# Kernel optimization log

Measured on AMD Instinct MI355X. Metric: run time of the kernel, lower is better.

The kernel has to match this reference:

```python
import jax, jax.numpy as jnp
import numpy as np

SEQ, D_IN, D_OUT = 4096, 1024, 1024


def setup_inputs() -> dict:
    key = jax.random.key(0)
    k_emb, k_q, k_k, k_v = jax.random.split(key, 4)
    # torch Linear stores weight as [out, in]; we keep [in, out] for x @ W
    scale = 1.0 / np.sqrt(D_IN)
    return {
        "embeddings": jax.random.normal(k_emb, (SEQ, D_IN), dtype=jnp.float32),
        "w_query": jax.random.uniform(k_q, (D_IN, D_OUT), dtype=jnp.float32, minval=-scale, maxval=scale),
        "w_key": jax.random.uniform(k_k, (D_IN, D_OUT), dtype=jnp.float32, minval=-scale, maxval=scale),
        "w_value": jax.random.uniform(k_v, (D_IN, D_OUT), dtype=jnp.float32, minval=-scale, maxval=scale),
    }


def reference(embeddings, w_query, w_key, w_value):
    # QKV projections (bias=False)
    q = embeddings @ w_query  # [S, D_out]
    k = embeddings @ w_key    # [S, D_out]
    v = embeddings @ w_value  # [S, D_out]
    inv_sqrt_d = 1.0 / jnp.sqrt(jnp.asarray(k.shape[-1], dtype=q.dtype))
    scores = jnp.einsum("sd,td->st", q, k) * inv_sqrt_d  # [S, S]
    weights = jax.nn.softmax(scores, axis=-1)
    return weights @ v  # [S, D_out]
```

## Files before the change

### kernel.cpp

```cpp
#include <hip/hip_runtime.h>
#include <hip/hip_bf16.h>

typedef unsigned short u16;
typedef __bf16 bf16x8 __attribute__((ext_vector_type(8)));
typedef float f32x4 __attribute__((ext_vector_type(4)));
typedef unsigned short u16x8 __attribute__((ext_vector_type(8)));
typedef unsigned short u16x4 __attribute__((ext_vector_type(4)));

__device__ __forceinline__ float bf2f(u16 u) {
  unsigned x = ((unsigned)u) << 16;
  return __builtin_bit_cast(float, x);
}
__device__ __forceinline__ u16 f2bf(float f) {
  unsigned u = __builtin_bit_cast(unsigned, f);
  u += 0x7fffu + ((u >> 16) & 1u);
  return (u16)(u >> 16);
}

__device__ __forceinline__ void gload16(const u16* g, u16* lds) {
  __builtin_amdgcn_global_load_lds(
      (const __attribute__((address_space(1))) void*)g,
      (__attribute__((address_space(3))) void*)lds,
      16, 0, 0);
}

template <int OUT_MODE, int NX, int BK>
__device__ __forceinline__ void gemm_body(
    const u16* __restrict__ A, int lda,
    const u16* __restrict__ B, int ldb,
    void* __restrict__ C, int ldc, int kt0, int Kc, float cscale,
    u16* As, u16* Bs, int bid)
{
  constexpr int CPR = BK / 8;
  constexpr int RPG = 512 / BK;
  constexpr int IPW = 32 / RPG;

  const int by = (bid & 7) + 8 * (bid / (8 * NX));
  const int bx = (bid >> 3) % NX;
  const int m0 = by * 128, n0 = bx * 128;

  const int t = threadIdx.x;
  const int w = t >> 6, l = t & 63;
  const int srow = l / CPR;
  const int lc = l % CPR;
  const int wm = (w >> 1) * 64, wn = (w & 1) * 64;
  const int fr = l & 15;
  const int q = l >> 4;

  f32x4 acc[4][4] = {};

  for (int kk = 0; kk < Kc; kk += BK) {
    const int kt = kt0 + kk;
    __syncthreads();
#pragma unroll
    for (int j = 0; j < IPW; ++j) {
      const int rr = RPG * (IPW * w + j);
      const int ga = rr + srow;
      const int sch = ((lc ^ (ga & 7))) * 8;
      gload16(A + (size_t)(m0 + ga) * lda + kt + sch, As + rr * BK);
      gload16(B + (size_t)(n0 + ga) * ldb + kt + sch, Bs + rr * BK);
    }
    __syncthreads();

#pragma unroll
    for (int s = 0; s < BK / 32; ++s) {
      const int j = s * 4 + q;
      bf16x8 af[4], bfr[4];
#pragma unroll
      for (int i = 0; i < 4; ++i) {
        const int ra = wm + 16 * i + fr;
        af[i] = *(const bf16x8*)(As + ra * BK + (j ^ (ra & 7)) * 8);
      }
#pragma unroll
      for (int i = 0; i < 4; ++i) {
        const int rb = wn + 16 * i + fr;
        bfr[i] = *(const bf16x8*)(Bs + rb * BK + (j ^ (rb & 7)) * 8);
      }
#pragma unroll
      for (int i = 0; i < 4; ++i)
#pragma unroll
        for (int jj = 0; jj < 4; ++jj)
          acc[i][jj] = __builtin_amdgcn_mfma_f32_16x16x32_bf16(af[i], bfr[jj], acc[i][jj], 0, 0, 0);
    }
  }

  const int er = q * 4;
  const int ec = l & 15;
#pragma unroll
  for (int i = 0; i < 4; ++i)
#pragma unroll
    for (int jj = 0; jj < 4; ++jj)
#pragma unroll
      for (int r = 0; r < 4; ++r) {
        const size_t idx = (size_t)(m0 + wm + 16 * i + er + r) * ldc + (n0 + wn + 16 * jj + ec);
        if (OUT_MODE == 1) ((u16*)C)[idx] = f2bf(acc[i][jj][r] * cscale);
        else               ((float*)C)[idx] = acc[i][jj][r];
      }
}

__global__ __launch_bounds__(256) void gemm_qkv(const u16* __restrict__ A,
                                                const u16* __restrict__ B,
                                                u16* __restrict__ C) {
  __shared__ __align__(16) u16 As[128 * 64], Bs[128 * 64];
  gemm_body<1, 24, 64>(A, 1024, B, 1024, C, 3072, 0, 1024, 1.0f, As, Bs, blockIdx.x);
}

__global__ __launch_bounds__(256) void score_tv(const u16* __restrict__ QKV,
                                                u16* __restrict__ S,
                                                u16* __restrict__ Vt) {
  __shared__ __align__(16) u16 As[128 * 64], Bs[128 * 64];
  const int b = blockIdx.x;
  if (b < 1024) {
    gemm_body<1, 32, 64>(QKV, 3072, QKV + 1024, 3072, S, 4096, 0, 1024,
                         0.03125f, As, Bs, b);
  } else {
    const int v = b - 1024;
    const int c0 = (v & 31) * 32;
    const int r0 = (v >> 5) * 32;
    u16 (*tl)[33] = (u16(*)[33])As;
    const int tx = threadIdx.x & 31, ty0 = threadIdx.x >> 5;
    const u16* Vin = QKV + 2048;
#pragma unroll
    for (int k = 0; k < 4; ++k) {
      const int ty = ty0 + k * 8;
      tl[ty][tx] = Vin[(size_t)(r0 + ty) * 3072 + c0 + tx];
    }
    __syncthreads();
#pragma unroll
    for (int k = 0; k < 4; ++k) {
      const int ty = ty0 + k * 8;
      Vt[(size_t)(c0 + ty) * 4096 + r0 + tx] = tl[tx][ty];
    }
  }
}

__global__ __launch_bounds__(256) void gemm_pv(const u16* __restrict__ S,
                                               const u16* __restrict__ Vt,
                                               float* __restrict__ O0,
                                               float* __restrict__ O1) {
  __shared__ __align__(16) u16 As[128 * 128], Bs[128 * 128];
  float* C = blockIdx.z ? O1 : O0;
  gemm_body<0, 8, 128>(S, 4096, Vt, 4096, C, 1024, blockIdx.z * 2048, 2048,
                       1.0f, As, Bs, blockIdx.x);
}

__global__ __launch_bounds__(256) void reduce_add(float4* __restrict__ out,
                                                  const float4* __restrict__ p) {
  const int i = blockIdx.x * 256 + threadIdx.x;
  float4 a = out[i], b = p[i];
  out[i] = float4{a.x + b.x, a.y + b.y, a.z + b.z, a.w + b.w};
}

__global__ __launch_bounds__(256) void prep(
    const float* __restrict__ E,
    const float* __restrict__ w0, const float* __restrict__ w1,
    const float* __restrict__ w2,
    u16* __restrict__ Ebf, u16* __restrict__ Wt)
{
  int b = blockIdx.x;
  if (b < 4096) {
    const int i = (b * 256 + threadIdx.x) * 4;
    float4 f = *(const float4*)(E + i);
    u16x4 o;
    o.x = f2bf(f.x); o.y = f2bf(f.y); o.z = f2bf(f.z); o.w = f2bf(f.w);
    *(u16x4*)(Ebf + i) = o;
  } else {
    b -= 4096;
    const int which = b >> 10;
    const int tile = b & 1023;
    const float* in = (which == 0) ? w0 : (which == 1) ? w1 : w2;
    u16* o = Wt + (size_t)which * 1024 * 1024;
    const int c0 = (tile & 31) * 32, r0 = (tile >> 5) * 32;
    __shared__ u16 tl[32][33];
    const int tx = threadIdx.x & 31, ty0 = threadIdx.x >> 5;
#pragma unroll
    for (int k = 0; k < 4; ++k) {
      const int ty = ty0 + k * 8;
      tl[ty][tx] = f2bf(in[(size_t)(r0 + ty) * 1024 + c0 + tx]);
    }
    __syncthreads();
#pragma unroll
    for (int k = 0; k < 4; ++k) {
      const int ty = ty0 + k * 8;
      o[(size_t)(c0 + ty) * 1024 + r0 + tx] = tl[tx][ty];
    }
  }
}

__global__ __launch_bounds__(256) void softmax_rows(u16* __restrict__ S) {
  const int N = 4096;
  u16* p = S + (size_t)blockIdx.x * N;
  const int t = threadIdx.x;
  u16x8 u0 = ((const u16x8*)p)[t * 2];
  u16x8 u1 = ((const u16x8*)p)[t * 2 + 1];
  float v[16];
#pragma unroll
  for (int i = 0; i < 8; ++i) v[i] = bf2f(u0[i]);
#pragma unroll
  for (int i = 0; i < 8; ++i) v[8 + i] = bf2f(u1[i]);

  float m = -1e30f;
#pragma unroll
  for (int i = 0; i < 16; ++i) m = fmaxf(m, v[i]);
#pragma unroll
  for (int off = 32; off; off >>= 1) m = fmaxf(m, __shfl_xor(m, off));
  __shared__ float red[8];
  if ((t & 63) == 0) red[t >> 6] = m;
  __syncthreads();
  m = fmaxf(fmaxf(red[0], red[1]), fmaxf(red[2], red[3]));

  float s = 0.f;
#pragma unroll
  for (int i = 0; i < 16; ++i) { v[i] = __expf(v[i] - m); s += v[i]; }
#pragma unroll
  for (int off = 32; off; off >>= 1) s += __shfl_xor(s, off);
  if ((t & 63) == 0) red[4 + (t >> 6)] = s;
  __syncthreads();
  s = (red[4] + red[5]) + (red[6] + red[7]);
  const float inv = 1.0f / s;

  u16x8 o0, o1;
#pragma unroll
  for (int i = 0; i < 8; ++i) o0[i] = f2bf(v[i] * inv);
#pragma unroll
  for (int i = 0; i < 8; ++i) o1[i] = f2bf(v[8 + i] * inv);
  ((u16x8*)p)[t * 2] = o0;
  ((u16x8*)p)[t * 2 + 1] = o1;
}

extern "C" void kernel_launch(void* const* d_in, const int* in_sizes, int n_in,
                              void* d_out, int out_size, void* d_ws, size_t ws_size,
                              hipStream_t stream) {
  const float* E  = (const float*)d_in[0];
  const float* Wq = (const float*)d_in[1];
  const float* Wk = (const float*)d_in[2];
  const float* Wv = (const float*)d_in[3];
  float* Out = (float*)d_out;

  char* w = (char*)d_ws;
  u16* Ebf = (u16*)(w);
  u16* Wt  = (u16*)(w + (size_t)(8u << 20));
  u16* QKV = (u16*)(w + (size_t)(14u << 20));
  u16* Vt  = (u16*)(w + (size_t)(38u << 20));
  u16* S   = (u16*)(w + (size_t)(46u << 20));
  float* P1 = (float*)(w);

  prep<<<7168, 256, 0, stream>>>(E, Wq, Wk, Wv, Ebf, Wt);

  gemm_qkv<<<768, 256, 0, stream>>>(Ebf, Wt, QKV);

  score_tv<<<5120, 256, 0, stream>>>(QKV, S, Vt);

  softmax_rows<<<4096, 256, 0, stream>>>(S);

  gemm_pv<<<dim3(256, 1, 2), 256, 0, stream>>>(S, Vt, Out, P1);
  reduce_add<<<4096, 256, 0, stream>>>((float4*)Out, (const float4*)P1);
}
```

Measured before the change: 220.0 us.

## Replace split-K PV GEMM with 128x64 tiles and drop reduce kernel

Generalizes the GEMM body to a configurable N-tile width and runs the P·V GEMM with 128x64 output tiles over the full K=4096 in 512 blocks, instead of split-K into two partial outputs. This removes the extra partial-sum write, the reduce_add kernel launch and its read-modify-write traffic. In exchange each block runs a longer K loop, and the narrower tile does fewer MFMAs per A-tile load, which lowers arithmetic intensity.

```diff
diff --git a/kernel.cpp b/kernel.cpp
--- a/kernel.cpp
+++ b/kernel.cpp
@@ -24,7 +24,7 @@
       16, 0, 0);
 }
 
-template <int OUT_MODE, int NX, int BK>
+template <int OUT_MODE, int NX, int BK, int BN>
 __device__ __forceinline__ void gemm_body(
     const u16* __restrict__ A, int lda,
     const u16* __restrict__ B, int ldb,
@@ -33,53 +33,62 @@
 {
   constexpr int CPR = BK / 8;
   constexpr int RPG = 512 / BK;
-  constexpr int IPW = 32 / RPG;
+  constexpr int IPA = 32 / RPG;
+  constexpr int IPB = (BN / 4) / RPG;
+  constexpr int NWN = BN / 32;
 
   const int by = (bid & 7) + 8 * (bid / (8 * NX));
   const int bx = (bid >> 3) % NX;
-  const int m0 = by * 128, n0 = bx * 128;
+  const int m0 = by * 128, n0 = bx * BN;
 
   const int t = threadIdx.x;
   const int w = t >> 6, l = t & 63;
   const int srow = l / CPR;
   const int lc = l % CPR;
-  const int wm = (w >> 1) * 64, wn = (w & 1) * 64;
+  const int wm = (w >> 1) * 64;
+  const int wn = (w & 1) * (BN / 2);
   const int fr = l & 15;
   const int q = l >> 4;
 
-  f32x4 acc[4][4] = {};
+  f32x4 acc[4][NWN] = {};
 
   for (int kk = 0; kk < Kc; kk += BK) {
     const int kt = kt0 + kk;
     __syncthreads();
 #pragma unroll
-    for (int j = 0; j < IPW; ++j) {
-      const int rr = RPG * (IPW * w + j);
+    for (int j = 0; j < IPA; ++j) {
+      const int rr = RPG * (IPA * w + j);
       const int ga = rr + srow;
       const int sch = ((lc ^ (ga & 7))) * 8;
       gload16(A + (size_t)(m0 + ga) * lda + kt + sch, As + rr * BK);
-      gload16(B + (size_t)(n0 + ga) * ldb + kt + sch, Bs + rr * BK);
+    }
+#pragma unroll
+    for (int j = 0; j < IPB; ++j) {
+      const int rr = RPG * (IPB * w + j);
+      const int gb = rr + srow;
+      const int sch = ((lc ^ (gb & 7))) * 8;
+      gload16(B + (size_t)(n0 + gb) * ldb + kt + sch, Bs + rr * BK);
     }
     __syncthreads();
 
 #pragma unroll
     for (int s = 0; s < BK / 32; ++s) {
       const int j = s * 4 + q;
-      bf16x8 af[4], bfr[4];
+      bf16x8 af[4], bfr[NWN];
 #pragma unroll
       for (int i = 0; i < 4; ++i) {
         const int ra = wm + 16 * i + fr;
         af[i] = *(const bf16x8*)(As + ra * BK + (j ^ (ra & 7)) * 8);
       }
 #pragma unroll
-      for (int i = 0; i < 4; ++i) {
+      for (int i = 0; i < NWN; ++i) {
         const int rb = wn + 16 * i + fr;
         bfr[i] = *(const bf16x8*)(Bs + rb * BK + (j ^ (rb & 7)) * 8);
       }
 #pragma unroll
       for (int i = 0; i < 4; ++i)
 #pragma unroll
-        for (int jj = 0; jj < 4; ++jj)
+        for (int jj = 0; jj < NWN; ++jj)
           acc[i][jj] = __builtin_amdgcn_mfma_f32_16x16x32_bf16(af[i], bfr[jj], acc[i][jj], 0, 0, 0);
     }
   }
@@ -89,7 +98,7 @@
 #pragma unroll
   for (int i = 0; i < 4; ++i)
 #pragma unroll
-    for (int jj = 0; jj < 4; ++jj)
+    for (int jj = 0; jj < NWN; ++jj)
 #pragma unroll
       for (int r = 0; r < 4; ++r) {
         const size_t idx = (size_t)(m0 + wm + 16 * i + er + r) * ldc + (n0 + wn + 16 * jj + ec);
@@ -102,7 +111,7 @@
                                                 const u16* __restrict__ B,
                                                 u16* __restrict__ C) {
   __shared__ __align__(16) u16 As[128 * 64], Bs[128 * 64];
-  gemm_body<1, 24, 64>(A, 1024, B, 1024, C, 3072, 0, 1024, 1.0f, As, Bs, blockIdx.x);
+  gemm_body<1, 24, 64, 128>(A, 1024, B, 1024, C, 3072, 0, 1024, 1.0f, As, Bs, blockIdx.x);
 }
 
 __global__ __launch_bounds__(256) void score_tv(const u16* __restrict__ QKV,
@@ -111,8 +120,8 @@
   __shared__ __align__(16) u16 As[128 * 64], Bs[128 * 64];
   const int b = blockIdx.x;
   if (b < 1024) {
-    gemm_body<1, 32, 64>(QKV, 3072, QKV + 1024, 3072, S, 4096, 0, 1024,
-                         0.03125f, As, Bs, b);
+    gemm_body<1, 32, 64, 128>(QKV, 3072, QKV + 1024, 3072, S, 4096, 0, 1024,
+                              0.03125f, As, Bs, b);
   } else {
     const int v = b - 1024;
     const int c0 = (v & 31) * 32;
@@ -136,19 +145,10 @@
 
 __global__ __launch_bounds__(256) void gemm_pv(const u16* __restrict__ S,
                                                const u16* __restrict__ Vt,
-                                               float* __restrict__ O0,
-                                               float* __restrict__ O1) {
-  __shared__ __align__(16) u16 As[128 * 128], Bs[128 * 128];
-  float* C = blockIdx.z ? O1 : O0;
-  gemm_body<0, 8, 128>(S, 4096, Vt, 4096, C, 1024, blockIdx.z * 2048, 2048,
-                       1.0f, As, Bs, blockIdx.x);
-}
-
-__global__ __launch_bounds__(256) void reduce_add(float4* __restrict__ out,
-                                                  const float4* __restrict__ p) {
-  const int i = blockIdx.x * 256 + threadIdx.x;
-  float4 a = out[i], b = p[i];
-  out[i] = float4{a.x + b.x, a.y + b.y, a.z + b.z, a.w + b.w};
+                                               float* __restrict__ O) {
+  __shared__ __align__(16) u16 As[128 * 128], Bs[64 * 128];
+  gemm_body<0, 16, 128, 64>(S, 4096, Vt, 4096, O, 1024, 0, 4096,
+                            1.0f, As, Bs, blockIdx.x);
 }
 
 __global__ __launch_bounds__(256) void prep(
@@ -243,7 +243,6 @@
   u16* QKV = (u16*)(w + (size_t)(14u << 20));
   u16* Vt  = (u16*)(w + (size_t)(38u << 20));
   u16* S   = (u16*)(w + (size_t)(46u << 20));
-  float* P1 = (float*)(w);
 
   prep<<<7168, 256, 0, stream>>>(E, Wq, Wk, Wv, Ebf, Wt);
 
@@ -253,6 +252,5 @@
 
   softmax_rows<<<4096, 256, 0, stream>>>(S);
 
-  gemm_pv<<<dim3(256, 1, 2), 256, 0, stream>>>(S, Vt, Out, P1);
-  reduce_add<<<4096, 256, 0, stream>>>((float4*)Out, (const float4*)P1);
-}
+  gemm_pv<<<512, 256, 0, stream>>>(S, Vt, Out);
+}
```

Result: no change. 217.5 us (-1.2%).
